# Performance work log

Hardware: AMD Instinct MI355X
Metric: run time of the kernel (lower is better)

The kernel has to match this reference:

```python
import jax, jax.numpy as jnp
import numpy as np

# dims: H heads, D=word_size (d_model), E=embed_dim per head, N=seq_len=n, K=linformer k
H, D, E, N, K = 16, 1024, 64, 4096, 256


def setup_inputs() -> dict:
    key = jax.random.key(0)
    ks = jax.random.split(key, 9)
    s = 0.02  # init scale for weights
    return {
        "x":  jax.random.normal(ks[0], (N, D), jnp.float32),
        # per-head QKV linears: torch Linear weight is (out=E, in=D), bias (E,)
        "Wq": jax.random.normal(ks[1], (H, E, D), jnp.float32) * s,
        "bq": jnp.zeros((H, E), jnp.float32),
        "Wk": jax.random.normal(ks[2], (H, E, D), jnp.float32) * s,
        "bk": jnp.zeros((H, E), jnp.float32),
        "Wv": jax.random.normal(ks[3], (H, E, D), jnp.float32) * s,
        "bv": jnp.zeros((H, E), jnp.float32),
        # per-head E/F sequence projections: Linear(n=N, k=K) -> weight (K, N), bias (K,)
        "Ew": jax.random.normal(ks[4], (H, K, N), jnp.float32) * s,
        "Eb": jnp.zeros((H, K), jnp.float32),
        "Fw": jax.random.normal(ks[5], (H, K, N), jnp.float32) * s,
        "Fb": jnp.zeros((H, K), jnp.float32),
        # output projection: Linear(H*E, E, bias=False) -> weight (E, H*E)
        "Wo": jax.random.normal(ks[6], (E, H * E), jnp.float32) * s,
    }


def reference(x, Wq, bq, Wk, bk, Wv, bv, Ew, Eb, Fw, Fb, Wo):
    # per-head Q/K/V projections, batched over heads: (H, N, E)
    q = jnp.einsum('nd,hed->hne', x, Wq) + bq[:, None, :]
    k = jnp.einsum('nd,hed->hne', x, Wk) + bk[:, None, :]
    v = jnp.einsum('nd,hed->hne', x, Wv) + bv[:, None, :]
    # low-rank sequence-length projection of K and V: (H, K, E)
    kp = jnp.einsum('hjn,hne->hje', Ew, k) + Eb[:, :, None]
    vp = jnp.einsum('hjn,hne->hje', Fw, v) + Fb[:, :, None]
    # scaled dot-product attention against projected keys: (H, N, K)
    score = jnp.einsum('hne,hje->hnj', q, kp) / jnp.sqrt(jnp.float32(E))
    attn = jax.nn.softmax(score, axis=-1)
    z = jnp.einsum('hnj,hje->hne', attn, vp)  # (H, N, E)
    # concat heads along feature dim (matches torch.cat(dim=1)): (N, H*E)
    zs = jnp.transpose(z, (1, 0, 2)).reshape(N, H * E)
    # final projection Linear(H*E, E, bias=False)
    return zs @ Wo.T  # (N, E)
```

## Files before the change

kernel.cpp:

```cpp
#include <hip/hip_runtime.h>
#include <hip/hip_bf16.h>

typedef __attribute__((ext_vector_type(4))) float f32x4;
typedef __attribute__((ext_vector_type(8))) short s16x8;
typedef __attribute__((ext_vector_type(4))) short s16x4;
typedef unsigned short u16;


__device__ __forceinline__ f32x4 mfma16(s16x8 a, s16x8 b, f32x4 c) {
    return __builtin_amdgcn_mfma_f32_16x16x32_bf16(a, b, c, 0, 0, 0);
}

__device__ __forceinline__ u16 bf(float f) {
    union { float f; unsigned u; } x; x.f = f;
    return (u16)((x.u + 0x7fffu + ((x.u >> 16) & 1u)) >> 16);
}
__device__ __forceinline__ unsigned pkbf(float a, float b) {
    union { float f; unsigned u; } x, y; x.f = a; y.f = b;
    unsigned ra = x.u + 0x7fffu + ((x.u >> 16) & 1u);
    unsigned rb = y.u + 0x7fffu + ((y.u >> 16) & 1u);
    return (ra >> 16) | (rb & 0xffff0000u);
}

__device__ __forceinline__ void gl_lds16(const u16* g, u16* l) {
    __builtin_amdgcn_global_load_lds(
        (const __attribute__((address_space(1))) unsigned*)g,
        (__attribute__((address_space(3))) unsigned*)l, 16, 0, 0);
}


__global__ __launch_bounds__(256) void cvt_all_kernel(
        const float* __restrict__ x,  const float* __restrict__ Wq,
        const float* __restrict__ Wk, const float* __restrict__ Wv,
        const float* __restrict__ Wo,
        u16* __restrict__ xb, u16* __restrict__ wb, u16* __restrict__ wob) {
    int i = blockIdx.x * 256 + threadIdx.x;
    const float* src; u16* dst; int off;
    if (i < 1048576)      { src = x;  dst = xb;            off = i; }
    else if (i < 1310720) { src = Wq; dst = wb;            off = i - 1048576; }
    else if (i < 1572864) { src = Wk; dst = wb + 1048576;  off = i - 1310720; }
    else if (i < 1835008) { src = Wv; dst = wb + 2097152;  off = i - 1572864; }
    else if (i < 1851392) { src = Wo; dst = wob;           off = i - 1835008; }
    else return;
    f32x4 v = ((const f32x4*)src)[off];
    union { s16x4 v; unsigned u[2]; } r;
    r.u[0] = pkbf(v.x, v.y);
    r.u[1] = pkbf(v.z, v.w);
    ((s16x4*)dst)[off] = r.v;
}


__global__ __launch_bounds__(256, 3) void qkv_kernel(
        const u16* __restrict__ xb, const u16* __restrict__ wb,
        const float* __restrict__ bq, const float* __restrict__ bk,
        const float* __restrict__ bv,
        u16* __restrict__ qo, u16* __restrict__ kTo, u16* __restrict__ vTo) {
    __shared__ u16 As[128 * 32];
    __shared__ u16 Bs[128 * 32];
    int bx   = blockIdx.x % 24;
    int by   = blockIdx.x / 24;
    int tid  = threadIdx.x;
    int lane = tid & 63, w = tid >> 6;
    int l15  = lane & 15, quad = lane >> 4;
    int wr   = w >> 1, wc = w & 1;

    const u16* Ag = xb + (size_t)(by * 128 + (tid >> 2)) * 1024 + (tid & 3) * 8;
    const u16* Bg = wb + (size_t)(bx * 128 + (tid >> 2)) * 1024 + (tid & 3) * 8;
    u16* Al = As + tid * 8;
    u16* Bl = Bs + tid * 8;

    const u16* abase = As + (wr * 64 + l15) * 32 + quad * 8;
    const u16* bbase = Bs + (wc * 64 + l15) * 32 + quad * 8;

    f32x4 acc[4][4] = {};
    for (int k0 = 0; k0 < 1024; k0 += 32) {
        gl_lds16(Ag + k0, Al);
        gl_lds16(Ag + 64 * 1024 + k0, Al + 64 * 32);
        gl_lds16(Bg + k0, Bl);
        gl_lds16(Bg + 64 * 1024 + k0, Bl + 64 * 32);
        __syncthreads();
        s16x8 a[4], b[4];
#pragma unroll
        for (int mi = 0; mi < 4; mi++) a[mi] = *(const s16x8*)(abase + mi * 16 * 32);
#pragma unroll
        for (int nj = 0; nj < 4; nj++) b[nj] = *(const s16x8*)(bbase + nj * 16 * 32);
#pragma unroll
        for (int mi = 0; mi < 4; mi++)
#pragma unroll
            for (int nj = 0; nj < 4; nj++) acc[mi][nj] = mfma16(a[mi], b[nj], acc[mi][nj]);
        __syncthreads();
    }

    int fblk = (bx * 128 + wc * 64) >> 6;
    int mat  = fblk >> 4, h = fblk & 15;
    const float* bias = (mat == 0) ? bq : (mat == 1 ? bk : bv);
#pragma unroll
    for (int nj = 0; nj < 4; nj++) {
        int e = nj * 16 + l15;
        float bb = bias[h * 64 + e];
#pragma unroll
        for (int mi = 0; mi < 4; mi++) {
            int n0 = by * 128 + wr * 64 + mi * 16 + quad * 4;
            f32x4 c = acc[mi][nj];
            if (mat == 0) {
                u16* p = qo + ((size_t)h * 4096 + n0) * 64 + e;
#pragma unroll
                for (int r = 0; r < 4; r++) p[(size_t)r * 64] = bf(c[r] + bb);
            } else {
                u16* p = (mat == 1 ? kTo : vTo) + ((size_t)h * 64 + e) * 4096 + n0;
                union { s16x4 v; u16 s[4]; } pk;
#pragma unroll
                for (int r = 0; r < 4; r++) pk.s[r] = bf(c[r] + bb);
                *(s16x4*)p = pk.v;
            }
        }
    }
}


__global__ __launch_bounds__(256, 2) void kpvp_kernel(
        const float* __restrict__ Ew, const float* __restrict__ Fw,
        const u16* __restrict__ kT, const u16* __restrict__ vT,
        float* __restrict__ accs) {
    int b    = blockIdx.x;
    int ks   = b & 15, h = (b >> 4) & 15, p = b >> 8;
    int tid  = threadIdx.x;
    int lane = tid & 63, w = tid >> 6;
    int l15  = lane & 15, quad = lane >> 4;

    const float* Ap = (p ? Fw : Ew)
        + (size_t)(h * 256 + w * 64 + l15) * 4096 + ks * 256 + quad * 8;
    const u16* Bp = (p ? vT : kT)
        + ((size_t)(h * 64 + l15)) * 4096 + ks * 256 + quad * 8;

    f32x4 acc[4][4] = {};
#pragma unroll 2
    for (int kk = 0; kk < 256; kk += 32) {
        s16x8 a[4], bb[4];
#pragma unroll
        for (int mt = 0; mt < 4; mt++) {
            f32x4 v0 = *(const f32x4*)(Ap + (size_t)mt * 16 * 4096 + kk);
            f32x4 v1 = *(const f32x4*)(Ap + (size_t)mt * 16 * 4096 + kk + 4);
            union { s16x8 q; unsigned u[4]; } r;
            r.u[0] = pkbf(v0.x, v0.y);
            r.u[1] = pkbf(v0.z, v0.w);
            r.u[2] = pkbf(v1.x, v1.y);
            r.u[3] = pkbf(v1.z, v1.w);
            a[mt] = r.q;
        }
#pragma unroll
        for (int nt = 0; nt < 4; nt++)
            bb[nt] = *(const s16x8*)(Bp + (size_t)nt * 16 * 4096 + kk);
#pragma unroll
        for (int mt = 0; mt < 4; mt++)
#pragma unroll
            for (int nt = 0; nt < 4; nt++)
                acc[mt][nt] = mfma16(a[mt], bb[nt], acc[mt][nt]);
    }

    size_t base = (size_t)ks * 524288
        + ((size_t)(p * 16 + h) * 256 + w * 64 + quad * 4) * 64 + l15;
#pragma unroll
    for (int mt = 0; mt < 4; mt++)
#pragma unroll
        for (int nt = 0; nt < 4; nt++)
#pragma unroll
            for (int r = 0; r < 4; r++)
                accs[base + (size_t)(mt * 16 + r) * 64 + nt * 16] = acc[mt][nt][r];
}


__global__ __launch_bounds__(256) void packkv_kernel(
        const float* __restrict__ accs, const float* __restrict__ Eb,
        const float* __restrict__ Fb, u16* __restrict__ kp, u16* __restrict__ vpT) {
    int idx = blockIdx.x * 256 + threadIdx.x;
    float v = 0.f;
#pragma unroll
    for (int s = 0; s < 16; s++) v += accs[idx + (size_t)s * 524288];
    int p = idx >> 18, h = (idx >> 14) & 15, j = (idx >> 6) & 255, e = idx & 63;
    if (p == 0) {
        v += Eb[h * 256 + j];
        kp[((size_t)(h * 256 + j)) * 64 + e] = bf(v * 0.125f);
    } else {
        v += Fb[h * 256 + j];
        vpT[((size_t)(h * 64 + e)) * 256 + j] = bf(v);
    }
}


__global__ __launch_bounds__(256) void attn_kernel(
        const u16* __restrict__ q, const u16* __restrict__ kp,
        const u16* __restrict__ vpT, u16* __restrict__ zs) {
    __shared__ u16 ps[4][16][256];
    int bm   = blockIdx.x & 63, h = blockIdx.x >> 6;
    int lane = threadIdx.x & 63, w = threadIdx.x >> 6;
    int l15  = lane & 15, quad = lane >> 4;
    int nbase = bm * 64 + w * 16;

    f32x4 s[16] = {};
    const u16* qp  = q  + ((size_t)h * 4096 + nbase + l15) * 64 + quad * 8;
    const u16* kpp = kp + ((size_t)h * 256 + l15) * 64 + quad * 8;
#pragma unroll
    for (int e0 = 0; e0 < 64; e0 += 32) {
        s16x8 a = *(const s16x8*)(qp + e0);
#pragma unroll
        for (int jt = 0; jt < 16; jt++) {
            s16x8 b = *(const s16x8*)(kpp + jt * 16 * 64 + e0);
            s[jt] = mfma16(a, b, s[jt]);
        }
    }

    float lsum[4];
#pragma unroll
    for (int r = 0; r < 4; r++) {
        float m = s[0][r];
#pragma unroll
        for (int jt = 1; jt < 16; jt++) m = fmaxf(m, s[jt][r]);
        m = fmaxf(m, __shfl_xor(m, 1));
        m = fmaxf(m, __shfl_xor(m, 2));
        m = fmaxf(m, __shfl_xor(m, 4));
        m = fmaxf(m, __shfl_xor(m, 8));
        float l = 0.f;
#pragma unroll
        for (int jt = 0; jt < 16; jt++) {
            float pv = __expf(s[jt][r] - m);
            s[jt][r] = pv;
            l += pv;
        }
        l += __shfl_xor(l, 1);
        l += __shfl_xor(l, 2);
        l += __shfl_xor(l, 4);
        l += __shfl_xor(l, 8);
        lsum[r] = l;
    }

#pragma unroll
    for (int jt = 0; jt < 16; jt++)
#pragma unroll
        for (int r = 0; r < 4; r++)
            ps[w][quad * 4 + r][jt * 16 + l15] = bf(s[jt][r]);
    __syncthreads();

    f32x4 z[4] = {};
    const u16* vp = vpT + ((size_t)h * 64 + l15) * 256 + quad * 8;
#pragma unroll
    for (int kj = 0; kj < 8; kj++) {
        s16x8 a = *(const s16x8*)&ps[w][l15][kj * 32 + quad * 8];
#pragma unroll
        for (int et = 0; et < 4; et++) {
            s16x8 b = *(const s16x8*)(vp + et * 16 * 256 + kj * 32);
            z[et] = mfma16(a, b, z[et]);
        }
    }
#pragma unroll
    for (int et = 0; et < 4; et++) {
        int e = et * 16 + l15;
        u16* o = zs + ((size_t)(nbase + quad * 4)) * 1024 + h * 64 + e;
#pragma unroll
        for (int r = 0; r < 4; r++) o[(size_t)r * 1024] = bf(z[et][r] / lsum[r]);
    }
}


__global__ __launch_bounds__(256) void out_kernel(
        const u16* __restrict__ zs, const u16* __restrict__ wob,
        float* __restrict__ oslice) {
    int ks   = blockIdx.x & 3;
    int bm   = blockIdx.x >> 2;
    int lane = threadIdx.x & 63, w = threadIdx.x >> 6;
    int l15  = lane & 15, quad = lane >> 4;
    int row0 = bm * 128 + w * 32;

    const u16* A = zs  + (size_t)(row0 + l15) * 1024 + ks * 256 + quad * 8;
    const u16* B = wob + (size_t)l15 * 1024 + ks * 256 + quad * 8;

    f32x4 acc[2][4] = {};
    for (int k = 0; k < 256; k += 32) {
        s16x8 a0 = *(const s16x8*)(A + k);
        s16x8 a1 = *(const s16x8*)(A + 16 * 1024 + k);
#pragma unroll
        for (int nt = 0; nt < 4; nt++) {
            s16x8 bv = *(const s16x8*)(B + (size_t)nt * 16 * 1024 + k);
            acc[0][nt] = mfma16(a0, bv, acc[0][nt]);
            acc[1][nt] = mfma16(a1, bv, acc[1][nt]);
        }
    }
    float* os = oslice + (size_t)ks * 262144;
#pragma unroll
    for (int mt = 0; mt < 2; mt++)
#pragma unroll
        for (int nt = 0; nt < 4; nt++) {
            int e = nt * 16 + l15;
            int n0 = row0 + mt * 16 + quad * 4;
            float* o = os + (size_t)n0 * 64 + e;
#pragma unroll
            for (int r = 0; r < 4; r++) o[(size_t)r * 64] = acc[mt][nt][r];
        }
}

__global__ __launch_bounds__(256) void outred_kernel(
        const float* __restrict__ oslice, float* __restrict__ out) {
    int i = blockIdx.x * 256 + threadIdx.x;
    out[i] = oslice[i] + oslice[i + 262144] + oslice[i + 524288] + oslice[i + 786432];
}


extern "C" void kernel_launch(void* const* d_in, const int* in_sizes, int n_in,
                              void* d_out, int out_size, void* d_ws, size_t ws_size,
                              hipStream_t stream) {
    const float* x  = (const float*)d_in[0];
    const float* Wq = (const float*)d_in[1];
    const float* bq = (const float*)d_in[2];
    const float* Wk = (const float*)d_in[3];
    const float* bk = (const float*)d_in[4];
    const float* Wv = (const float*)d_in[5];
    const float* bv = (const float*)d_in[6];
    const float* Ew = (const float*)d_in[7];
    const float* Eb = (const float*)d_in[8];
    const float* Fw = (const float*)d_in[9];
    const float* Fb = (const float*)d_in[10];
    const float* Wo = (const float*)d_in[11];

    char* ws = (char*)d_ws;
    u16*   qb   = (u16*)(ws + 0);
    u16*   kT   = (u16*)(ws + 8388608);
    u16*   vT   = (u16*)(ws + 16777216);
    u16*   zsb  = (u16*)(ws + 25165824);
    float* accs = (float*)(ws + 33554432);
    u16*   kp   = (u16*)(ws + 67108864);
    u16*   vpT  = (u16*)(ws + 67633152);
    u16*   xb   = (u16*)(ws + 68157440);
    u16*   wb   = (u16*)(ws + 76546048);
    u16*   wob  = (u16*)(ws + 82837504);

    cvt_all_kernel<<<7232, 256, 0, stream>>>(x, Wq, Wk, Wv, Wo, xb, wb, wob);
    qkv_kernel<<<768, 256, 0, stream>>>(xb, wb, bq, bk, bv, qb, kT, vT);
    kpvp_kernel<<<512, 256, 0, stream>>>(Ew, Fw, kT, vT, accs);
    packkv_kernel<<<2048, 256, 0, stream>>>(accs, Eb, Fb, kp, vpT);
    attn_kernel<<<1024, 256, 0, stream>>>(qb, kp, vpT, zsb);
    out_kernel<<<128, 256, 0, stream>>>(zsb, wob, (float*)accs);
    outred_kernel<<<1024, 256, 0, stream>>>((const float*)accs, (float*)d_out);
}
```

Before: 298.8 us.

## Stage kpvp operands through double-buffered LDS with async global-to-LDS loads

Rewrites the Linformer E/F projection kernel to stream fp32 Ew/Fw tiles and bf16 K/V tiles into double-buffered, XOR-swizzled shared memory using global_load_lds, with explicit vmcnt waits and barriers. It also halves the per-block row tile, doubling the grid to 1024 blocks and raising the occupancy hint. The aim is to hide global load latency and replace strided direct global loads with coalesced loads. In exchange it adds barrier overhead, halves per-block work, and the occupancy hint of 4 may tighten register limits.

```diff
diff --git a/kernel.cpp b/kernel.cpp
--- a/kernel.cpp
+++ b/kernel.cpp
@@ -22,7 +22,7 @@
     return (ra >> 16) | (rb & 0xffff0000u);
 }
 
-__device__ __forceinline__ void gl_lds16(const u16* g, u16* l) {
+__device__ __forceinline__ void gl_lds16(const void* g, void* l) {
     __builtin_amdgcn_global_load_lds(
         (const __attribute__((address_space(1))) unsigned*)g,
         (__attribute__((address_space(3))) unsigned*)l, 16, 0, 0);
@@ -118,50 +118,79 @@
 }
 
 
-__global__ __launch_bounds__(256, 2) void kpvp_kernel(
+__global__ __launch_bounds__(256, 4) void kpvp_kernel(
         const float* __restrict__ Ew, const float* __restrict__ Fw,
         const u16* __restrict__ kT, const u16* __restrict__ vT,
         float* __restrict__ accs) {
+    __shared__ float As[2][4096];
+    __shared__ u16  Bs[2][2048];
     int b    = blockIdx.x;
-    int ks   = b & 15, h = (b >> 4) & 15, p = b >> 8;
+    int ks   = b & 15, jb = (b >> 4) & 1, h = (b >> 5) & 15, p = b >> 9;
     int tid  = threadIdx.x;
     int lane = tid & 63, w = tid >> 6;
     int l15  = lane & 15, quad = lane >> 4;
 
-    const float* Ap = (p ? Fw : Ew)
-        + (size_t)(h * 256 + w * 64 + l15) * 4096 + ks * 256 + quad * 8;
-    const u16* Bp = (p ? vT : kT)
-        + ((size_t)(h * 64 + l15)) * 4096 + ks * 256 + quad * 8;
-
-    f32x4 acc[4][4] = {};
-#pragma unroll 2
-    for (int kk = 0; kk < 256; kk += 32) {
-        s16x8 a[4], bb[4];
-#pragma unroll
-        for (int mt = 0; mt < 4; mt++) {
-            f32x4 v0 = *(const f32x4*)(Ap + (size_t)mt * 16 * 4096 + kk);
-            f32x4 v1 = *(const f32x4*)(Ap + (size_t)mt * 16 * 4096 + kk + 4);
-            union { s16x8 q; unsigned u[4]; } r;
-            r.u[0] = pkbf(v0.x, v0.y);
-            r.u[1] = pkbf(v0.z, v0.w);
-            r.u[2] = pkbf(v1.x, v1.y);
-            r.u[3] = pkbf(v1.z, v1.w);
-            a[mt] = r.q;
+    int arow = tid >> 3, aslot = tid & 7;
+    const float* Asrc = (p ? Fw : Ew)
+        + (size_t)(h * 256 + jb * 128 + arow) * 4096 + ks * 256
+        + ((aslot ^ (arow & 7)) << 2);
+    int brow = tid >> 2, bslot = tid & 3;
+    const u16* Bsrc = (p ? vT : kT)
+        + (size_t)(h * 64 + brow) * 4096 + ks * 256
+        + ((bslot ^ (brow & 3)) << 3);
+
+    auto STAGE = [&](int it, int buf) {
+        int k0 = it * 32;
+#pragma unroll
+        for (int r = 0; r < 4; r++)
+            gl_lds16(Asrc + (size_t)r * 131072 + k0, &As[buf][r * 1024 + tid * 4]);
+        gl_lds16(Bsrc + k0, &Bs[buf][tid * 8]);
+    };
+
+    STAGE(0, 0);
+    STAGE(1, 1);
+
+    int r0 = w * 32 + l15;
+    int swa = l15 & 7, swb = l15 & 3;
+    f32x4 acc[2][4] = {};
+#pragma unroll
+    for (int it = 0; it < 8; ++it) {
+        if (it < 7) asm volatile("s_waitcnt vmcnt(5)" ::: "memory");
+        else        asm volatile("s_waitcnt vmcnt(0)" ::: "memory");
+        __builtin_amdgcn_s_barrier();
+        asm volatile("" ::: "memory");
+        const float* ab = As[it & 1];
+        const u16*  bbf = Bs[it & 1];
+        s16x8 a[2], bb[4];
+#pragma unroll
+        for (int mt = 0; mt < 2; mt++) {
+            const float* ap = ab + (size_t)(r0 + mt * 16) * 32;
+            f32x4 v0 = *(const f32x4*)(ap + (((2 * quad)     ^ swa) << 2));
+            f32x4 v1 = *(const f32x4*)(ap + (((2 * quad + 1) ^ swa) << 2));
+            union { s16x8 q; unsigned u[4]; } rr;
+            rr.u[0] = pkbf(v0.x, v0.y);
+            rr.u[1] = pkbf(v0.z, v0.w);
+            rr.u[2] = pkbf(v1.x, v1.y);
+            rr.u[3] = pkbf(v1.z, v1.w);
+            a[mt] = rr.q;
         }
 #pragma unroll
         for (int nt = 0; nt < 4; nt++)
-            bb[nt] = *(const s16x8*)(Bp + (size_t)nt * 16 * 4096 + kk);
-#pragma unroll
-        for (int mt = 0; mt < 4; mt++)
+            bb[nt] = *(const s16x8*)(bbf + (nt * 16 + l15) * 32 + ((quad ^ swb) << 3));
+#pragma unroll
+        for (int mt = 0; mt < 2; mt++)
 #pragma unroll
             for (int nt = 0; nt < 4; nt++)
                 acc[mt][nt] = mfma16(a[mt], bb[nt], acc[mt][nt]);
+        asm volatile("" ::: "memory");
+        __builtin_amdgcn_s_barrier();
+        if (it < 6) STAGE(it + 2, it & 1);
     }
 
     size_t base = (size_t)ks * 524288
-        + ((size_t)(p * 16 + h) * 256 + w * 64 + quad * 4) * 64 + l15;
-#pragma unroll
-    for (int mt = 0; mt < 4; mt++)
+        + ((size_t)(p * 16 + h) * 256 + jb * 128 + w * 32 + quad * 4) * 64 + l15;
+#pragma unroll
+    for (int mt = 0; mt < 2; mt++)
 #pragma unroll
         for (int nt = 0; nt < 4; nt++)
 #pragma unroll
@@ -335,7 +364,7 @@
 
     cvt_all_kernel<<<7232, 256, 0, stream>>>(x, Wq, Wk, Wv, Wo, xb, wb, wob);
     qkv_kernel<<<768, 256, 0, stream>>>(xb, wb, bq, bk, bv, qb, kT, vT);
-    kpvp_kernel<<<512, 256, 0, stream>>>(Ew, Fw, kT, vT, accs);
+    kpvp_kernel<<<1024, 256, 0, stream>>>(Ew, Fw, kT, vT, accs);
     packkv_kernel<<<2048, 256, 0, stream>>>(accs, Eb, Fb, kp, vpT);
     attn_kernel<<<1024, 256, 0, stream>>>(qb, kp, vpT, zsb);
     out_kernel<<<128, 256, 0, stream>>>(zsb, wob, (float*)accs);
```

After: 298.0 us. Within noise of the previous version (-0.2%).

## Split kpvp work per wave into 16-row tiles with register double-buffering

Applied to the files above, without the earlier changes.

The kpvp kernel now gives each wave its own 16-row j-tile instead of each block covering 64 rows per wave. The grid grows from 512 to 2048 blocks and per-wave accumulators shrink from 16 to 4. The loop is also software-pipelined: the next k-slice of Ew/Fw and kT/vT is prefetched into registers while the current slice is converted and multiplied. This aims to raise occupancy and hide global-load latency, at the cost of reloading each B tile once per j-tile, which is 4x more kT/vT traffic.

```diff
diff --git a/kernel.cpp b/kernel.cpp
--- a/kernel.cpp
+++ b/kernel.cpp
@@ -22,7 +22,7 @@
     return (ra >> 16) | (rb & 0xffff0000u);
 }
 
-__device__ __forceinline__ void gl_lds16(const u16* g, u16* l) {
+__device__ __forceinline__ void gl_lds16(const void* g, void* l) {
     __builtin_amdgcn_global_load_lds(
         (const __attribute__((address_space(1))) unsigned*)g,
         (__attribute__((address_space(3))) unsigned*)l, 16, 0, 0);
@@ -118,55 +118,57 @@
 }
 
 
-__global__ __launch_bounds__(256, 2) void kpvp_kernel(
+__global__ __launch_bounds__(256) void kpvp_kernel(
         const float* __restrict__ Ew, const float* __restrict__ Fw,
         const u16* __restrict__ kT, const u16* __restrict__ vT,
         float* __restrict__ accs) {
-    int b    = blockIdx.x;
-    int ks   = b & 15, h = (b >> 4) & 15, p = b >> 8;
     int tid  = threadIdx.x;
-    int lane = tid & 63, w = tid >> 6;
-    int l15  = lane & 15, quad = lane >> 4;
+    int w = tid >> 6, lane = tid & 63;
+    int l15 = lane & 15, quad = lane >> 4;
+    int gw = blockIdx.x * 4 + w;
+    int ks = gw & 15, jt = (gw >> 4) & 15, h = (gw >> 8) & 15, p = gw >> 12;
 
     const float* Ap = (p ? Fw : Ew)
-        + (size_t)(h * 256 + w * 64 + l15) * 4096 + ks * 256 + quad * 8;
+        + (size_t)(h * 256 + jt * 16 + l15) * 4096 + ks * 256 + quad * 8;
     const u16* Bp = (p ? vT : kT)
-        + ((size_t)(h * 64 + l15)) * 4096 + ks * 256 + quad * 8;
-
-    f32x4 acc[4][4] = {};
-#pragma unroll 2
-    for (int kk = 0; kk < 256; kk += 32) {
-        s16x8 a[4], bb[4];
-#pragma unroll
-        for (int mt = 0; mt < 4; mt++) {
-            f32x4 v0 = *(const f32x4*)(Ap + (size_t)mt * 16 * 4096 + kk);
-            f32x4 v1 = *(const f32x4*)(Ap + (size_t)mt * 16 * 4096 + kk + 4);
-            union { s16x8 q; unsigned u[4]; } r;
-            r.u[0] = pkbf(v0.x, v0.y);
-            r.u[1] = pkbf(v0.z, v0.w);
-            r.u[2] = pkbf(v1.x, v1.y);
-            r.u[3] = pkbf(v1.z, v1.w);
-            a[mt] = r.q;
-        }
-#pragma unroll
-        for (int nt = 0; nt < 4; nt++)
-            bb[nt] = *(const s16x8*)(Bp + (size_t)nt * 16 * 4096 + kk);
-#pragma unroll
-        for (int mt = 0; mt < 4; mt++)
-#pragma unroll
-            for (int nt = 0; nt < 4; nt++)
-                acc[mt][nt] = mfma16(a[mt], bb[nt], acc[mt][nt]);
+        + (size_t)(h * 64 + l15) * 4096 + ks * 256 + quad * 8;
+
+    f32x4 acc[4] = {};
+    f32x4 ca0 = *(const f32x4*)(Ap);
+    f32x4 ca1 = *(const f32x4*)(Ap + 4);
+    s16x8 cb0 = *(const s16x8*)(Bp);
+    s16x8 cb1 = *(const s16x8*)(Bp + 1 * 16 * 4096);
+    s16x8 cb2 = *(const s16x8*)(Bp + 2 * 16 * 4096);
+    s16x8 cb3 = *(const s16x8*)(Bp + 3 * 16 * 4096);
+#pragma unroll
+    for (int it = 0; it < 8; ++it) {
+        int kn = (it < 7) ? (it + 1) * 32 : 0;
+        f32x4 na0 = *(const f32x4*)(Ap + kn);
+        f32x4 na1 = *(const f32x4*)(Ap + kn + 4);
+        s16x8 nb0 = *(const s16x8*)(Bp + kn);
+        s16x8 nb1 = *(const s16x8*)(Bp + 1 * 16 * 4096 + kn);
+        s16x8 nb2 = *(const s16x8*)(Bp + 2 * 16 * 4096 + kn);
+        s16x8 nb3 = *(const s16x8*)(Bp + 3 * 16 * 4096 + kn);
+        union { s16x8 q; unsigned u[4]; } rr;
+        rr.u[0] = pkbf(ca0.x, ca0.y);
+        rr.u[1] = pkbf(ca0.z, ca0.w);
+        rr.u[2] = pkbf(ca1.x, ca1.y);
+        rr.u[3] = pkbf(ca1.z, ca1.w);
+        acc[0] = mfma16(rr.q, cb0, acc[0]);
+        acc[1] = mfma16(rr.q, cb1, acc[1]);
+        acc[2] = mfma16(rr.q, cb2, acc[2]);
+        acc[3] = mfma16(rr.q, cb3, acc[3]);
+        ca0 = na0; ca1 = na1;
+        cb0 = nb0; cb1 = nb1; cb2 = nb2; cb3 = nb3;
     }
 
     size_t base = (size_t)ks * 524288
-        + ((size_t)(p * 16 + h) * 256 + w * 64 + quad * 4) * 64 + l15;
-#pragma unroll
-    for (int mt = 0; mt < 4; mt++)
-#pragma unroll
-        for (int nt = 0; nt < 4; nt++)
-#pragma unroll
-            for (int r = 0; r < 4; r++)
-                accs[base + (size_t)(mt * 16 + r) * 64 + nt * 16] = acc[mt][nt][r];
+        + ((size_t)(p * 16 + h) * 256 + jt * 16 + quad * 4) * 64 + l15;
+#pragma unroll
+    for (int nt = 0; nt < 4; nt++)
+#pragma unroll
+        for (int r = 0; r < 4; r++)
+            accs[base + (size_t)r * 64 + nt * 16] = acc[nt][r];
 }
 
 
@@ -335,7 +337,7 @@
 
     cvt_all_kernel<<<7232, 256, 0, stream>>>(x, Wq, Wk, Wv, Wo, xb, wb, wob);
     qkv_kernel<<<768, 256, 0, stream>>>(xb, wb, bq, bk, bv, qb, kT, vT);
-    kpvp_kernel<<<512, 256, 0, stream>>>(Ew, Fw, kT, vT, accs);
+    kpvp_kernel<<<2048, 256, 0, stream>>>(Ew, Fw, kT, vT, accs);
     packkv_kernel<<<2048, 256, 0, stream>>>(accs, Eb, Fb, kp, vpT);
     attn_kernel<<<1024, 256, 0, stream>>>(qb, kp, vpT, zsb);
     out_kernel<<<128, 256, 0, stream>>>(zsb, wob, (float*)accs);
```

Result: slower. 316.6 us (+6.0%).

## Reduce kpvp split-K partials via in-block LDS reduction and swizzle attn LDS

Applied to the files above, without the earlier changes.

The kpvp kernel is restructured into 512-thread blocks in which four waves split the sequence dimension. Their partial tiles are summed through shared memory, so each block writes one reduced tile and only two split-K partials reach global memory instead of sixteen. This cuts global write and read traffic for the partials, and packkv now sums two slices instead of sixteen. The attention kernel's probability tile in LDS also gets an XOR swizzle to avoid bank conflicts, at the cost of an extra sync and about 70KB of LDS per kpvp block, which limits occupancy.

```diff
diff --git a/kernel.cpp b/kernel.cpp
--- a/kernel.cpp
+++ b/kernel.cpp
@@ -22,7 +22,7 @@
     return (ra >> 16) | (rb & 0xffff0000u);
 }
 
-__device__ __forceinline__ void gl_lds16(const u16* g, u16* l) {
+__device__ __forceinline__ void gl_lds16(const void* g, void* l) {
     __builtin_amdgcn_global_load_lds(
         (const __attribute__((address_space(1))) unsigned*)g,
         (__attribute__((address_space(3))) unsigned*)l, 16, 0, 0);
@@ -118,55 +118,72 @@
 }
 
 
-__global__ __launch_bounds__(256, 2) void kpvp_kernel(
+__global__ __launch_bounds__(512) void kpvp_kernel(
         const float* __restrict__ Ew, const float* __restrict__ Fw,
         const u16* __restrict__ kT, const u16* __restrict__ vT,
         float* __restrict__ accs) {
+    __shared__ float Ls[8][32][68];
     int b    = blockIdx.x;
-    int ks   = b & 15, h = (b >> 4) & 15, p = b >> 8;
+    int ks   = b & 1, jb = (b >> 1) & 3, h = (b >> 3) & 15, p = b >> 7;
     int tid  = threadIdx.x;
-    int lane = tid & 63, w = tid >> 6;
+    int w    = tid >> 6, lane = tid & 63;
+    int wj   = w >> 2, wk = w & 3;
     int l15  = lane & 15, quad = lane >> 4;
 
     const float* Ap = (p ? Fw : Ew)
-        + (size_t)(h * 256 + w * 64 + l15) * 4096 + ks * 256 + quad * 8;
+        + (size_t)(h * 256 + jb * 64 + wj * 32 + l15) * 4096
+        + ks * 2048 + wk * 512 + quad * 8;
     const u16* Bp = (p ? vT : kT)
-        + ((size_t)(h * 64 + l15)) * 4096 + ks * 256 + quad * 8;
-
-    f32x4 acc[4][4] = {};
+        + (size_t)(h * 64 + l15) * 4096 + ks * 2048 + wk * 512 + quad * 8;
+
+    f32x4 acc[2][4] = {};
 #pragma unroll 2
-    for (int kk = 0; kk < 256; kk += 32) {
-        s16x8 a[4], bb[4];
-#pragma unroll
-        for (int mt = 0; mt < 4; mt++) {
+    for (int kk = 0; kk < 512; kk += 32) {
+        s16x8 a[2], bb[4];
+#pragma unroll
+        for (int mt = 0; mt < 2; mt++) {
             f32x4 v0 = *(const f32x4*)(Ap + (size_t)mt * 16 * 4096 + kk);
             f32x4 v1 = *(const f32x4*)(Ap + (size_t)mt * 16 * 4096 + kk + 4);
-            union { s16x8 q; unsigned u[4]; } r;
-            r.u[0] = pkbf(v0.x, v0.y);
-            r.u[1] = pkbf(v0.z, v0.w);
-            r.u[2] = pkbf(v1.x, v1.y);
-            r.u[3] = pkbf(v1.z, v1.w);
-            a[mt] = r.q;
+            union { s16x8 q; unsigned u[4]; } rr;
+            rr.u[0] = pkbf(v0.x, v0.y);
+            rr.u[1] = pkbf(v0.z, v0.w);
+            rr.u[2] = pkbf(v1.x, v1.y);
+            rr.u[3] = pkbf(v1.z, v1.w);
+            a[mt] = rr.q;
         }
 #pragma unroll
         for (int nt = 0; nt < 4; nt++)
             bb[nt] = *(const s16x8*)(Bp + (size_t)nt * 16 * 4096 + kk);
 #pragma unroll
-        for (int mt = 0; mt < 4; mt++)
+        for (int mt = 0; mt < 2; mt++)
 #pragma unroll
             for (int nt = 0; nt < 4; nt++)
                 acc[mt][nt] = mfma16(a[mt], bb[nt], acc[mt][nt]);
     }
 
+#pragma unroll
+    for (int mt = 0; mt < 2; mt++)
+#pragma unroll
+        for (int nt = 0; nt < 4; nt++)
+#pragma unroll
+            for (int r = 0; r < 4; r++)
+                Ls[w][mt * 16 + quad * 4 + r][nt * 16 + l15] = acc[mt][nt][r];
+    __syncthreads();
+
+    int jl = tid >> 3, e0 = (tid & 7) * 8;
+    int wjr = jl >> 5, j32 = jl & 31;
+    f32x4 s0 = {}, s1 = {};
+#pragma unroll
+    for (int sk = 0; sk < 4; sk++) {
+        const float* Lp = &Ls[wjr * 4 + sk][j32][e0];
+        s0 += *(const f32x4*)Lp;
+        s1 += *(const f32x4*)(Lp + 4);
+    }
+    int jg = jb * 64 + jl;
     size_t base = (size_t)ks * 524288
-        + ((size_t)(p * 16 + h) * 256 + w * 64 + quad * 4) * 64 + l15;
-#pragma unroll
-    for (int mt = 0; mt < 4; mt++)
-#pragma unroll
-        for (int nt = 0; nt < 4; nt++)
-#pragma unroll
-            for (int r = 0; r < 4; r++)
-                accs[base + (size_t)(mt * 16 + r) * 64 + nt * 16] = acc[mt][nt][r];
+        + ((size_t)(p * 16 + h) * 256 + jg) * 64 + e0;
+    *(f32x4*)(accs + base)     = s0;
+    *(f32x4*)(accs + base + 4) = s1;
 }
 
 
@@ -174,9 +191,7 @@
         const float* __restrict__ accs, const float* __restrict__ Eb,
         const float* __restrict__ Fb, u16* __restrict__ kp, u16* __restrict__ vpT) {
     int idx = blockIdx.x * 256 + threadIdx.x;
-    float v = 0.f;
-#pragma unroll
-    for (int s = 0; s < 16; s++) v += accs[idx + (size_t)s * 524288];
+    float v = accs[idx] + accs[idx + 524288];
     int p = idx >> 18, h = (idx >> 14) & 15, j = (idx >> 6) & 255, e = idx & 63;
     if (p == 0) {
         v += Eb[h * 256 + j];
@@ -237,15 +252,17 @@
 #pragma unroll
     for (int jt = 0; jt < 16; jt++)
 #pragma unroll
-        for (int r = 0; r < 4; r++)
-            ps[w][quad * 4 + r][jt * 16 + l15] = bf(s[jt][r]);
+        for (int r = 0; r < 4; r++) {
+            int row = quad * 4 + r;
+            ps[w][row][(jt * 16 + l15) ^ ((row & 7) << 3)] = bf(s[jt][r]);
+        }
     __syncthreads();
 
     f32x4 z[4] = {};
     const u16* vp = vpT + ((size_t)h * 64 + l15) * 256 + quad * 8;
 #pragma unroll
     for (int kj = 0; kj < 8; kj++) {
-        s16x8 a = *(const s16x8*)&ps[w][l15][kj * 32 + quad * 8];
+        s16x8 a = *(const s16x8*)&ps[w][l15][(kj * 32 + quad * 8) ^ ((l15 & 7) << 3)];
 #pragma unroll
         for (int et = 0; et < 4; et++) {
             s16x8 b = *(const s16x8*)(vp + et * 16 * 256 + kj * 32);
@@ -335,7 +352,7 @@
 
     cvt_all_kernel<<<7232, 256, 0, stream>>>(x, Wq, Wk, Wv, Wo, xb, wb, wob);
     qkv_kernel<<<768, 256, 0, stream>>>(xb, wb, bq, bk, bv, qb, kT, vT);
-    kpvp_kernel<<<512, 256, 0, stream>>>(Ew, Fw, kT, vT, accs);
+    kpvp_kernel<<<256, 512, 0, stream>>>(Ew, Fw, kT, vT, accs);
     packkv_kernel<<<2048, 256, 0, stream>>>(accs, Eb, Fb, kp, vpT);
     attn_kernel<<<1024, 256, 0, stream>>>(qb, kp, vpT, zsb);
     out_kernel<<<128, 256, 0, stream>>>(zsb, wob, (float*)accs);
```

Result: no change. 293.3 us (-1.8%).
